# Optimization experiments

Measured on AMD Instinct MI355X. Metric: run time of the kernel, lower is better.

## Reference

```python
import jax, jax.numpy as jnp
import numpy as np

# RBF_Conv2d config (matches init_kwargs)
KH = KW = 3
STRIDE = 1
OUT_CH = 256
IN_CH = 64
STD = 2.0  # gauss RBF std (activate_param[0])


def setup_inputs() -> dict:
    key = jax.random.key(0)
    k1, k2 = jax.random.split(key)
    x = jax.random.normal(k1, (16, IN_CH, 56, 56), dtype=jnp.float32)
    # kaiming_uniform_ on fan_in = IN_CH*KH*KW = 576 -> bound = sqrt(6/576)
    bound = float(np.sqrt(6.0 / (IN_CH * KH * KW)))
    weight = jax.random.uniform(k2, (OUT_CH, IN_CH * KH * KW), dtype=jnp.float32,
                                minval=-bound, maxval=bound)
    return {"x": x, "weight": weight}


def _cdist_conv(x, weight):
    # im2col: [B, C*KH*KW, Ho, Wo]; channel ordering (c, kh, kw) matches F.unfold
    patches = jax.lax.conv_general_dilated_patches(
        x, (KH, KW), (STRIDE, STRIDE), 'VALID')
    B, Kdim, Ho, Wo = patches.shape
    win = patches.reshape(B, Kdim, Ho * Wo).transpose(0, 2, 1)  # [B, P, K]
    # Euclidean distance via the expansion ||w||^2 + ||c||^2 - 2 w.c (no [B,P,K,O] tensor)
    w2 = jnp.sum(win * win, axis=-1, keepdims=True)            # [B, P, 1]
    c2 = jnp.sum(weight * weight, axis=-1)[None, None, :]      # [1, 1, O]
    d2 = w2 + c2 - 2.0 * jnp.einsum('bpk,ok->bpo', win, weight)
    dist = jnp.sqrt(jnp.maximum(d2, 1e-12))                    # [B, P, O]
    return dist, (B, Ho, Wo)


def reference(x, weight):
    dist, (B, Ho, Wo) = _cdist_conv(x, weight)
    # gauss RBF: exp(-d^2 / (2*std^2))
    act = jnp.exp(-(dist * dist) / (2.0 * STD * STD))
    # permute back to [B, O, Ho, Wo] like the torch code
    return act.transpose(0, 2, 1).reshape(B, OUT_CH, Ho, Wo)
```

## Files before the change

kernel.cpp:

```cpp
#include <hip/hip_runtime.h>
#include <hip/hip_bf16.h>
#include <stdint.h>

#define BATCH 16
#define IN_CH 64
#define HIN 56
#define WIN_ 56
#define HO 54
#define WO 54
#define P_PER_B (HO*WO)
#define P_PAD 2944
#define OUT_CH 256
#define KDIM 576
#define NPIX (HIN*WIN_)

typedef __attribute__((ext_vector_type(8))) short short8;
typedef __attribute__((ext_vector_type(4))) float f32x4;

__device__ __forceinline__ unsigned short f2bf(float f) {
    unsigned int u = __float_as_uint(f);
    unsigned int r = (u + 0x7fffu + ((u >> 16) & 1u)) >> 16;
    return (unsigned short)r;
}


__global__ void prep_weight(const float* __restrict__ w, short* __restrict__ wbf2,
                            float* __restrict__ c2) {
    int o = blockIdx.x;
    int lane = threadIdx.x;
    int ng = o >> 4, nl = o & 15;
    float s = 0.f;
    #pragma unroll
    for (int j = 0; j < 9; ++j) {
        int k = j * 64 + lane;
        int c = k / 9, tap = k % 9;
        float v = w[o * KDIM + k];
        s += v * v;
        int ks = c >> 5, qd = (c >> 3) & 3, cl = c & 7;
        ((unsigned short*)wbf2)[((((ng * 9 + tap) * 2 + ks) * 4 + qd) * 16 + nl) * 8 + cl]
            = f2bf(v);
    }
    #pragma unroll
    for (int off = 32; off > 0; off >>= 1) s += __shfl_down(s, off);
    if (lane == 0) c2[o] = s;
}

__global__ __launch_bounds__(256) void transpose_kernel(
    const float* __restrict__ x, short* __restrict__ xT, float* __restrict__ s) {
    __shared__ short lds[64 * 65];
    __shared__ float red[256];
    const int b    = blockIdx.x / 49;
    const int pix0 = (blockIdx.x % 49) * 64;
    const int tid  = threadIdx.x;
    const int quarter = tid >> 6;
    const int pix  = tid & 63;
    const float* xb = x + (size_t)b * IN_CH * NPIX + pix0 + pix;
    float acc = 0.f;
    #pragma unroll
    for (int it = 0; it < 16; ++it) {
        int c = quarter * 16 + it;
        float v = xb[c * NPIX];
        acc += v * v;
        lds[pix * 65 + c] = (short)f2bf(v);
    }
    red[tid] = acc;
    __syncthreads();
    const int cs = tid & 63;
    short* xTb = xT + ((size_t)b * NPIX + pix0) * 64;
    #pragma unroll
    for (int it = 0; it < 16; ++it) {
        int pixs = quarter * 16 + it;
        xTb[(size_t)pixs * 64 + cs] = lds[pixs * 65 + cs];
    }
    if (tid < 64)
        s[b * NPIX + pix0 + tid] = red[tid] + red[64 + tid] + red[128 + tid] + red[192 + tid];
}

__global__ void w2_kernel(const float* __restrict__ s, float* __restrict__ w2) {
    int t = blockIdx.x * 256 + threadIdx.x;
    if (t >= BATCH * P_PER_B) return;
    int b = t / P_PER_B, p = t % P_PER_B;
    int oh = p / WO, ow = p % WO;
    const float* sp = s + b * NPIX + oh * WIN_ + ow;
    float acc = 0.f;
    #pragma unroll
    for (int kh = 0; kh < 3; ++kh)
        #pragma unroll
        for (int kw = 0; kw < 3; ++kw)
            acc += sp[kh * WIN_ + kw];
    w2[b * P_PAD + p] = acc;
}


__global__ __launch_bounds__(64, 2) void gemm_rbf(
    const short* __restrict__ xT, const short* __restrict__ wbf2,
    const float* __restrict__ w2, const float* __restrict__ c2,
    float* __restrict__ out) {
    constexpr int dtab[9] = {0, 1, 2, 56, 57, 58, 112, 113, 114};
    __shared__ __align__(16) short ldsA[184 * 72];

    const int bx = blockIdx.x;
    const int b  = bx & 15;
    const int p0 = (bx >> 4) * 64;
    const int n0 = blockIdx.y * 64;

    const int lane = threadIdx.x;
    const int r16  = lane & 15;
    const int quad = lane >> 4;

    const int q0 = p0 + 2 * (p0 / WO);
    const short* g = xT + ((size_t)b * NPIX + q0) * 64;
    #pragma unroll
    for (int i = 0; i < 23; ++i) {
        int c = i * 64 + lane;
        short8 v = *(const short8*)(g + c * 8);
        int q = c >> 3, ch = c & 7;
        *(short8*)(ldsA + q * 72 + ch * 8) = v;
    }

    int qr[4];
    #pragma unroll
    for (int ms = 0; ms < 4; ++ms) {
        int p = p0 + ms * 16 + r16;
        if (p > P_PER_B - 1) p = P_PER_B - 1;
        qr[ms] = (p + 2 * (p / WO)) - q0;
    }

    const short* bb = wbf2 + (size_t)(n0 >> 4) * 9 * 2 * 512 + lane * 8;

    f32x4 acc[4][4];
    #pragma unroll
    for (int i = 0; i < 4; ++i)
        #pragma unroll
        for (int j = 0; j < 4; ++j)
            acc[i][j] = (f32x4){0.f, 0.f, 0.f, 0.f};

    short8 Bf[2][4][2];
    #pragma unroll
    for (int ns = 0; ns < 4; ++ns)
        #pragma unroll
        for (int ks = 0; ks < 2; ++ks)
            Bf[0][ns][ks] = *(const short8*)(bb + (ns * 9 * 2 + ks) * 512);

    #pragma unroll
    for (int t = 0; t < 9; ++t) {
        const int cur = t & 1, nxt = cur ^ 1;
        if (t < 8) {
            #pragma unroll
            for (int ns = 0; ns < 4; ++ns)
                #pragma unroll
                for (int ks = 0; ks < 2; ++ks)
                    Bf[nxt][ns][ks] =
                        *(const short8*)(bb + ((ns * 9 + t + 1) * 2 + ks) * 512);
        }
        short8 af[4][2];
        #pragma unroll
        for (int ms = 0; ms < 4; ++ms) {
            int rowb = (qr[ms] + dtab[t]) * 72;
            #pragma unroll
            for (int ks = 0; ks < 2; ++ks)
                af[ms][ks] = *(const short8*)(ldsA + rowb + (ks * 4 + quad) * 8);
        }
        #pragma unroll
        for (int ks = 0; ks < 2; ++ks)
            #pragma unroll
            for (int ms = 0; ms < 4; ++ms)
                #pragma unroll
                for (int ns = 0; ns < 4; ++ns)
                    acc[ms][ns] = __builtin_amdgcn_mfma_f32_16x16x32_bf16(
                        af[ms][ks], Bf[cur][ns][ks], acc[ms][ns], 0, 0, 0);
    }

    #pragma unroll
    for (int ms = 0; ms < 4; ++ms) {
        int p = p0 + ms * 16 + quad * 4;
        if (p >= P_PER_B) continue;
        f32x4 w2v = *(const f32x4*)(w2 + b * P_PAD + p);
        bool full = (p + 3 < P_PER_B);
        #pragma unroll
        for (int ns = 0; ns < 4; ++ns) {
            int o = n0 + ns * 16 + r16;
            float c2o = c2[o];
            f32x4 v;
            #pragma unroll
            for (int r = 0; r < 4; ++r) {
                float d2 = w2v[r] + c2o - 2.0f * acc[ms][ns][r];
                d2 = fmaxf(d2, 1e-12f);
                v[r] = __expf(-0.125f * d2);
            }
            float* outp = out + ((size_t)(b * OUT_CH + o)) * P_PER_B + p;
            if (full) {
                *(f32x4*)outp = v;
            } else {
                #pragma unroll
                for (int r = 0; r < 4; ++r)
                    if (p + r < P_PER_B) outp[r] = v[r];
            }
        }
    }
}


extern "C" void kernel_launch(void* const* d_in, const int* in_sizes, int n_in,
                              void* d_out, int out_size, void* d_ws, size_t ws_size,
                              hipStream_t stream) {
    const float* x = (const float*)d_in[0];
    const float* w = (const float*)d_in[1];
    float* out = (float*)d_out;

    char* ws = (char*)d_ws;
    const size_t wbf_bytes = (size_t)OUT_CH * KDIM * 2;
    const size_t c2_bytes  = 1024;
    const size_t w2_bytes  = (size_t)BATCH * P_PAD * 4;
    const size_t s_bytes   = (size_t)BATCH * NPIX * 4;
    short* wbf2 = (short*)ws;
    float* c2  = (float*)(ws + wbf_bytes);
    float* w2  = (float*)(ws + wbf_bytes + c2_bytes);
    float* s   = (float*)(ws + wbf_bytes + c2_bytes + w2_bytes);
    short* xT  = (short*)(ws + wbf_bytes + c2_bytes + w2_bytes + s_bytes);

    hipLaunchKernelGGL(prep_weight, dim3(OUT_CH), dim3(64), 0, stream, w, wbf2, c2);
    hipLaunchKernelGGL(transpose_kernel, dim3(16 * 49), dim3(256), 0, stream, x, xT, s);
    hipLaunchKernelGGL(w2_kernel, dim3((BATCH * P_PER_B + 255) / 256), dim3(256), 0, stream, s, w2);
    hipLaunchKernelGGL(gemm_rbf, dim3(46 * BATCH, OUT_CH / 64), dim3(64), 0, stream,
                       xT, wbf2, w2, c2, out);
}
```

Measured before the change: 107.5 us.

## Restructure RBF GEMM into persistent 4-wave blocks with LDS-resident weights and double-buffered A

The GEMM kernel becomes a 256-thread block that loads its whole 64-channel weight slice into LDS once via global_load_lds. It then loops over several 128-pixel tiles, double-buffering the im2col input window in LDS and using an XOR swizzle to avoid bank conflicts. This removes the repeated per-block weight fetches from global memory and overlaps input loads with MFMA work. In exchange it uses a large dynamic LDS footprint (about 135 KB, one block per CU) and a smaller grid of 512 blocks, which may leave CUs underused or unevenly loaded.

Result: no change. 109.4 us (+1.8%).

```diff
diff --git a/kernel.cpp b/kernel.cpp
--- a/kernel.cpp
+++ b/kernel.cpp
@@ -14,6 +14,13 @@
 #define KDIM 576
 #define NPIX (HIN*WIN_)
 
+#define NTILES_M 23
+#define CHUNKS 8
+#define BSLICE_SH 36864
+#define ABUF_SH 15872
+#define AWIN_GROUPS 31
+#define LDS_BYTES ((BSLICE_SH + 2*ABUF_SH) * 2)
+
 typedef __attribute__((ext_vector_type(8))) short short8;
 typedef __attribute__((ext_vector_type(4))) float f32x4;
 
@@ -92,111 +99,133 @@
 }
 
 
-__global__ __launch_bounds__(64, 2) void gemm_rbf(
+#define AS1(p) ((const __attribute__((address_space(1))) void*)(p))
+#define AS3(p) ((__attribute__((address_space(3))) void*)(p))
+
+__global__ __launch_bounds__(256, 1) void gemm_rbf(
     const short* __restrict__ xT, const short* __restrict__ wbf2,
     const float* __restrict__ w2, const float* __restrict__ c2,
     float* __restrict__ out) {
     constexpr int dtab[9] = {0, 1, 2, 56, 57, 58, 112, 113, 114};
-    __shared__ __align__(16) short ldsA[184 * 72];
-
-    const int bx = blockIdx.x;
-    const int b  = bx & 15;
-    const int p0 = (bx >> 4) * 64;
-    const int n0 = blockIdx.y * 64;
-
-    const int lane = threadIdx.x;
+    extern __shared__ __align__(16) short lds[];
+    short* ldsB = lds;
+
+    const int chunk = blockIdx.x;
+    const int ng    = blockIdx.y;
+    const int b     = blockIdx.z;
+
+    const int tid  = threadIdx.x;
+    const int wave = tid >> 6;
+    const int lane = tid & 63;
     const int r16  = lane & 15;
     const int quad = lane >> 4;
-
-    const int q0 = p0 + 2 * (p0 / WO);
-    const short* g = xT + ((size_t)b * NPIX + q0) * 64;
-    #pragma unroll
-    for (int i = 0; i < 23; ++i) {
-        int c = i * 64 + lane;
-        short8 v = *(const short8*)(g + c * 8);
-        int q = c >> 3, ch = c & 7;
-        *(short8*)(ldsA + q * 72 + ch * 8) = v;
-    }
-
-    int qr[4];
-    #pragma unroll
-    for (int ms = 0; ms < 4; ++ms) {
-        int p = p0 + ms * 16 + r16;
-        if (p > P_PER_B - 1) p = P_PER_B - 1;
-        qr[ms] = (p + 2 * (p / WO)) - q0;
-    }
-
-    const short* bb = wbf2 + (size_t)(n0 >> 4) * 9 * 2 * 512 + lane * 8;
-
-    f32x4 acc[4][4];
-    #pragma unroll
-    for (int i = 0; i < 4; ++i)
-        #pragma unroll
-        for (int j = 0; j < 4; ++j)
-            acc[i][j] = (f32x4){0.f, 0.f, 0.f, 0.f};
-
-    short8 Bf[2][4][2];
-    #pragma unroll
-    for (int ns = 0; ns < 4; ++ns)
-        #pragma unroll
-        for (int ks = 0; ks < 2; ++ks)
-            Bf[0][ns][ks] = *(const short8*)(bb + (ns * 9 * 2 + ks) * 512);
-
-    #pragma unroll
-    for (int t = 0; t < 9; ++t) {
-        const int cur = t & 1, nxt = cur ^ 1;
-        if (t < 8) {
+    const int srow = lane >> 3;
+    const int soff = srow * 128 + ((lane & 7) ^ srow) * 16;
+
+    const char* xTb = (const char*)(xT + (size_t)b * NPIX * 64);
+
+    const char* bsrc = (const char*)(wbf2 + (size_t)ng * BSLICE_SH) + lane * 16;
+    for (int g = wave; g < 72; g += 4)
+        __builtin_amdgcn_global_load_lds(AS1(bsrc + g * 1024), AS3(ldsB + g * 512), 16, 0, 0);
+
+    {
+        int p0 = chunk * 128;
+        int q0 = p0 + 2 * (p0 / WO);
+        const char* wb = xTb + (size_t)q0 * 128;
+        for (int g = wave; g < AWIN_GROUPS; g += 4)
+            __builtin_amdgcn_global_load_lds(AS1(wb + g * 1024 + soff),
+                                             AS3(lds + BSLICE_SH + g * 512), 16, 0, 0);
+    }
+    __syncthreads();
+
+    int i = 0;
+    for (int t = chunk; t < NTILES_M; t += CHUNKS, ++i) {
+        const int p0 = t * 128;
+        const int q0 = p0 + 2 * (p0 / WO);
+        const short* A = lds + BSLICE_SH + (i & 1) * ABUF_SH;
+
+        if (t + CHUNKS < NTILES_M) {
+            int p0n = (t + CHUNKS) * 128;
+            int q0n = p0n + 2 * (p0n / WO);
+            const char* wb = xTb + (size_t)q0n * 128;
+            short* dst = lds + BSLICE_SH + ((i + 1) & 1) * ABUF_SH;
+            for (int g = wave; g < AWIN_GROUPS; g += 4)
+                __builtin_amdgcn_global_load_lds(AS1(wb + g * 1024 + soff),
+                                                 AS3(dst + g * 512), 16, 0, 0);
+        }
+
+        int qr[2];
+        #pragma unroll
+        for (int ms = 0; ms < 2; ++ms) {
+            int p = p0 + wave * 32 + ms * 16 + r16;
+            if (p > P_PER_B - 1) p = P_PER_B - 1;
+            qr[ms] = (p + 2 * (p / WO)) - q0;
+        }
+
+        f32x4 acc[2][4];
+        #pragma unroll
+        for (int ms = 0; ms < 2; ++ms)
             #pragma unroll
             for (int ns = 0; ns < 4; ++ns)
+                acc[ms][ns] = (f32x4){0.f, 0.f, 0.f, 0.f};
+
+        #pragma unroll
+        for (int tap = 0; tap < 9; ++tap) {
+            short8 af[2][2], bf[4][2];
+            #pragma unroll
+            for (int ms = 0; ms < 2; ++ms) {
+                int row = qr[ms] + dtab[tap];
+                const short* aRow = A + row * 64;
+                int key = row & 7;
                 #pragma unroll
                 for (int ks = 0; ks < 2; ++ks)
-                    Bf[nxt][ns][ks] =
-                        *(const short8*)(bb + ((ns * 9 + t + 1) * 2 + ks) * 512);
-        }
-        short8 af[4][2];
-        #pragma unroll
-        for (int ms = 0; ms < 4; ++ms) {
-            int rowb = (qr[ms] + dtab[t]) * 72;
+                    af[ms][ks] = *(const short8*)(aRow + (((ks * 4 + quad) ^ key) * 8));
+            }
+            #pragma unroll
+            for (int ns = 0; ns < 4; ++ns)
+                #pragma unroll
+                for (int ks = 0; ks < 2; ++ks)
+                    bf[ns][ks] = *(const short8*)(ldsB + ns * 9216 + lane * 8
+                                                  + (tap * 2 + ks) * 512);
             #pragma unroll
             for (int ks = 0; ks < 2; ++ks)
-                af[ms][ks] = *(const short8*)(ldsA + rowb + (ks * 4 + quad) * 8);
-        }
-        #pragma unroll
-        for (int ks = 0; ks < 2; ++ks)
-            #pragma unroll
-            for (int ms = 0; ms < 4; ++ms)
-                #pragma unroll
-                for (int ns = 0; ns < 4; ++ns)
-                    acc[ms][ns] = __builtin_amdgcn_mfma_f32_16x16x32_bf16(
-                        af[ms][ks], Bf[cur][ns][ks], acc[ms][ns], 0, 0, 0);
-    }
-
-    #pragma unroll
-    for (int ms = 0; ms < 4; ++ms) {
-        int p = p0 + ms * 16 + quad * 4;
-        if (p >= P_PER_B) continue;
-        f32x4 w2v = *(const f32x4*)(w2 + b * P_PAD + p);
-        bool full = (p + 3 < P_PER_B);
-        #pragma unroll
-        for (int ns = 0; ns < 4; ++ns) {
-            int o = n0 + ns * 16 + r16;
-            float c2o = c2[o];
-            f32x4 v;
-            #pragma unroll
-            for (int r = 0; r < 4; ++r) {
-                float d2 = w2v[r] + c2o - 2.0f * acc[ms][ns][r];
-                d2 = fmaxf(d2, 1e-12f);
-                v[r] = __expf(-0.125f * d2);
+                #pragma unroll
+                for (int ms = 0; ms < 2; ++ms)
+                    #pragma unroll
+                    for (int ns = 0; ns < 4; ++ns)
+                        acc[ms][ns] = __builtin_amdgcn_mfma_f32_16x16x32_bf16(
+                            af[ms][ks], bf[ns][ks], acc[ms][ns], 0, 0, 0);
+        }
+
+        #pragma unroll
+        for (int ms = 0; ms < 2; ++ms) {
+            int p = p0 + wave * 32 + ms * 16 + quad * 4;
+            if (p < P_PER_B) {
+                f32x4 w2v = *(const f32x4*)(w2 + b * P_PAD + p);
+                bool full = (p + 3 < P_PER_B);
+                #pragma unroll
+                for (int ns = 0; ns < 4; ++ns) {
+                    int o = ng * 64 + ns * 16 + r16;
+                    float c2o = c2[o];
+                    f32x4 v;
+                    #pragma unroll
+                    for (int r = 0; r < 4; ++r) {
+                        float d2 = w2v[r] + c2o - 2.0f * acc[ms][ns][r];
+                        d2 = fmaxf(d2, 1e-12f);
+                        v[r] = __expf(-0.125f * d2);
+                    }
+                    float* outp = out + ((size_t)(b * OUT_CH + o)) * P_PER_B + p;
+                    if (full) {
+                        *(f32x4*)outp = v;
+                    } else {
+                        #pragma unroll
+                        for (int r = 0; r < 4; ++r)
+                            if (p + r < P_PER_B) outp[r] = v[r];
+                    }
+                }
             }
-            float* outp = out + ((size_t)(b * OUT_CH + o)) * P_PER_B + p;
-            if (full) {
-                *(f32x4*)outp = v;
-            } else {
-                #pragma unroll
-                for (int r = 0; r < 4; ++r)
-                    if (p + r < P_PER_B) outp[r] = v[r];
-            }
-        }
+        }
+        __syncthreads();
     }
 }
 
@@ -219,9 +248,12 @@
     float* s   = (float*)(ws + wbf_bytes + c2_bytes + w2_bytes);
     short* xT  = (short*)(ws + wbf_bytes + c2_bytes + w2_bytes + s_bytes);
 
+    (void)hipFuncSetAttribute((const void*)gemm_rbf,
+                              hipFuncAttributeMaxDynamicSharedMemorySize, LDS_BYTES);
+
     hipLaunchKernelGGL(prep_weight, dim3(OUT_CH), dim3(64), 0, stream, w, wbf2, c2);
     hipLaunchKernelGGL(transpose_kernel, dim3(16 * 49), dim3(256), 0, stream, x, xT, s);
     hipLaunchKernelGGL(w2_kernel, dim3((BATCH * P_PER_B + 255) / 256), dim3(256), 0, stream, s, w2);
-    hipLaunchKernelGGL(gemm_rbf, dim3(46 * BATCH, OUT_CH / 64), dim3(64), 0, stream,
+    hipLaunchKernelGGL(gemm_rbf, dim3(CHUNKS, 4, BATCH), dim3(256), LDS_BYTES, stream,
                        xT, wbf2, w2, c2, out);
 }
```
